# Kernel optimization log

Hardware: AMD Instinct MI355X
Metric: run time of the kernel (lower is better)

Reference implementation:

```python
import jax, jax.numpy as jnp
import numpy as np

NUM_EMBEDDINGS = 1024
EMBEDDING_DIM = 256
COMMITMENT_COST = 0.25
N_TOKENS = 65536


def setup_inputs() -> dict:
    key = jax.random.key(0)
    k1, k2 = jax.random.split(key)
    z = jax.random.normal(k1, (N_TOKENS, EMBEDDING_DIM), dtype=jnp.float32)
    # codebook init as in the module: uniform in [-1/K, 1/K]
    embedding = jax.random.uniform(
        k2, (NUM_EMBEDDINGS, EMBEDDING_DIM),
        minval=-1.0 / NUM_EMBEDDINGS, maxval=1.0 / NUM_EMBEDDINGS,
        dtype=jnp.float32)
    return {"z": z, "embedding": embedding}


def reference(z, embedding):
    # squared euclidean distances: ||z||^2 + ||e||^2 - 2 z.e^T   -> [N, K]
    z_sq = jnp.sum(z ** 2, axis=1, keepdims=True)          # [N, 1]
    emb_sq = jnp.sum(embedding ** 2, axis=1)               # [K]
    dot = jnp.dot(z, embedding.T)                          # [N, K]
    distances = z_sq + emb_sq - 2.0 * dot
    indices = jnp.argmin(distances, axis=1)                # [N]
    z_q = embedding[indices]                               # [N, D] gather
    loss = (jnp.mean((jax.lax.stop_gradient(z) - z_q) ** 2)
            + COMMITMENT_COST * jnp.mean((jax.lax.stop_gradient(z_q) - z) ** 2))
    z_q_st = z + jax.lax.stop_gradient(z_q - z)            # straight-through
    return (z_q_st, loss, indices)
```

## Files before the change

### kernel.cpp

```cpp
#include <hip/hip_runtime.h>
#include <hip/hip_bf16.h>

#define NTOK   65536
#define KCODES 1024
#define DIM    256
#define LOSS_OFF ((size_t)NTOK * DIM)
#define IDX_OFF  (LOSS_OFF + 1)

#define MARGA 2e-4f

#define SC_ZSQ    0
#define SC_LOSS2  131072
#define SC_ESQ    196608
#define SC_ESQNH  197632
#define SC_PART   198656
#define SC_WCNT   198720
#define SC_WCNT2  198721
#define SC_CNTG   198784
#define SC_LISTS  264320
#define SC_WLIST  788608
#define SC_WLIST2 854144
#define SC_EHIMG  858240
#define SC_ZIMG   989312
#define SC_PAIRD  9377920

typedef __attribute__((ext_vector_type(8))) short short8;
typedef __attribute__((ext_vector_type(4))) float f32x4;

__device__ __forceinline__ unsigned f2bf(float x) {
    unsigned u = __float_as_uint(x);
    return (u + 0x7FFFu + ((u >> 16) & 1u)) >> 16;
}

__device__ __forceinline__ void gload16(const void* g, void* l) {
    __builtin_amdgcn_global_load_lds((const __attribute__((address_space(1))) unsigned int*)g,
                                     (__attribute__((address_space(3))) unsigned int*)l,
                                     16, 0, 0);
}

__device__ __forceinline__ float faithful_d(const float* __restrict__ z,
                                            const float* __restrict__ emb,
                                            float zsq, float esq, int tok, int c) {
    const float4* zr = (const float4*)(z + (size_t)tok * DIM);
    const float4* er = (const float4*)(emb + (size_t)c * DIM);
    float acc = 0.f;
#pragma unroll 8
    for (int q = 0; q < 64; ++q) {
        float4 a = zr[q], b = er[q];
        acc = fmaf(a.x, b.x, acc); acc = fmaf(a.y, b.y, acc);
        acc = fmaf(a.z, b.z, acc); acc = fmaf(a.w, b.w, acc);
    }
    float t1 = zsq + esq;
    return t1 - 2.0f * acc;
}

__device__ __forceinline__ float np_rowsq256_wave(const float* row, int sub) {
    const int j = sub & 7, half = sub >> 3;
    const float* a = row + half * 128 + j;
    float r = 0.f;
#pragma unroll
    for (int i = 0; i < 16; ++i) {
        float v = a[i * 8];
        float sq = v * v;
        asm volatile("" : "+v"(sq));
        r += sq;
    }
    float t = r + __shfl_xor(r, 1, 64);
    t = t + __shfl_xor(t, 2, 64);
    t = t + __shfl_xor(t, 4, 64);
    t = t + __shfl_xor(t, 8, 64);
    return t;
}

__global__ __launch_bounds__(256) void vq_prep_esq(const float* __restrict__ emb,
                                                   float* __restrict__ esq,
                                                   float* __restrict__ esqnh,
                                                   int* __restrict__ wcnt,
                                                   int* __restrict__ wcnt2) {
    if (blockIdx.x == 0 && threadIdx.x == 0) { *wcnt = 0; *wcnt2 = 0; }
    int code = blockIdx.x * 16 + (threadIdx.x >> 4);
    int sub = threadIdx.x & 15;
    float tot = np_rowsq256_wave(emb + (size_t)code * DIM, sub);
    if (sub == 0) { esq[code] = tot; esqnh[code] = -0.5f * tot; }
}

__global__ __launch_bounds__(256) void vq_prep_z(const float* __restrict__ z,
                                                 float* __restrict__ zsq,
                                                 unsigned short* __restrict__ zimg) {
    int tok = blockIdx.x * 16 + (threadIdx.x >> 4);
    int sub = threadIdx.x & 15;
    float tot = np_rowsq256_wave(z + (size_t)tok * DIM, sub);
    if (sub == 0) zsq[tok] = tot;

    const float* src = z + (size_t)tok * DIM + sub * 16;
    float4 v0 = *(const float4*)&src[0],  v1 = *(const float4*)&src[4];
    float4 v2 = *(const float4*)&src[8],  v3 = *(const float4*)&src[12];
    uint4 p0, p1;
    p0.x = f2bf(v0.x) | (f2bf(v0.y) << 16);  p0.y = f2bf(v0.z) | (f2bf(v0.w) << 16);
    p0.z = f2bf(v1.x) | (f2bf(v1.y) << 16);  p0.w = f2bf(v1.z) | (f2bf(v1.w) << 16);
    p1.x = f2bf(v2.x) | (f2bf(v2.y) << 16);  p1.y = f2bf(v2.z) | (f2bf(v2.w) << 16);
    p1.z = f2bf(v3.x) | (f2bf(v3.y) << 16);  p1.w = f2bf(v3.z) | (f2bf(v3.w) << 16);

    int bid = tok >> 6, tf = (tok >> 4) & 3, sl = tok & 15;
    int g0 = sub * 2, g1 = g0 + 1;
    size_t rowbase = ((size_t)bid * 4 + tf) * 8;
    char* d0 = (char*)zimg + ((rowbase + (g0 >> 2)) << 10) + (((g0 & 3) * 16 + sl) << 4);
    char* d1 = (char*)zimg + ((rowbase + (g1 >> 2)) << 10) + (((g1 & 3) * 16 + sl) << 4);
    *(uint4*)d0 = p0;
    *(uint4*)d1 = p1;
}

__global__ __launch_bounds__(256) void vq_prep_eimg(const float* __restrict__ emb,
                                                    unsigned short* __restrict__ img) {
    int job = blockIdx.x * 256 + threadIdx.x;
    int code = job >> 3, ks = job & 7;
    int cc = (code >> 6) & 3, lcl = (code >> 8) * 64 + (code & 63);
    const float* src = emb + (size_t)code * DIM + ks * 32;
    char* base = (char*)img + (size_t)(cc * 8 + ks) * 16384;
#pragma unroll
    for (int q = 0; q < 4; ++q) {
        float4 v0 = *(const float4*)&src[q * 8];
        float4 v1 = *(const float4*)&src[q * 8 + 4];
        uint4 p;
        p.x = f2bf(v0.x) | (f2bf(v0.y) << 16);
        p.y = f2bf(v0.z) | (f2bf(v0.w) << 16);
        p.z = f2bf(v1.x) | (f2bf(v1.y) << 16);
        p.w = f2bf(v1.z) | (f2bf(v1.w) << 16);
        *(uint4*)(base + lcl * 64 + ((q * 16) ^ (((lcl >> 1) & 3) << 4))) = p;
    }
}

__global__ __launch_bounds__(256, 2) void vq_gemm(const unsigned short* __restrict__ zimg,
                                                  const unsigned short* __restrict__ img,
                                                  const float* __restrict__ esqnh,
                                                  const float* __restrict__ zsq,
                                                  int* __restrict__ wcnt,
                                                  int* __restrict__ wlist,
                                                  int* __restrict__ cntg,
                                                  int* __restrict__ listsg,
                                                  float* __restrict__ loss2,
                                                  float* __restrict__ dout) {
    __shared__ __align__(16) short eh_s[2][8192];
    __shared__ float a1w_s[4][64];
    __shared__ int   cnt_s[64];
    __shared__ int   lists_s[64 * 16];
    __shared__ float avals_s[64 * 16];

    const int tid = threadIdx.x, bid = blockIdx.x;
    const int w = tid >> 6, l = tid & 63;
    const int t0 = bid * 64;

    short8 zf[4][8];
#pragma unroll
    for (int tf = 0; tf < 4; ++tf)
#pragma unroll
        for (int ks = 0; ks < 8; ++ks)
            zf[tf][ks] = *(const short8*)((const char*)zimg +
                           ((((size_t)bid * 4 + tf) * 8 + ks) << 10) + (size_t)l * 16);

    if (tid < 64) cnt_s[tid] = 0;
    {
        const char* gs = (const char*)img + w * 4096 + (size_t)l * 16;
        char* ld = (char*)&eh_s[0][0] + w * 4096;
#pragma unroll
        for (int i = 0; i < 4; ++i) gload16(gs + i * 1024, ld + i * 1024);
    }
    __syncthreads();

    float m_run[4] = {-3.4e38f, -3.4e38f, -3.4e38f, -3.4e38f};
    f32x4 acc[4][4];

#pragma unroll
    for (int c = 0; c < 4; ++c) {
#pragma unroll
        for (int f = 0; f < 4; ++f) {
            f32x4 e4 = *(const f32x4*)&esqnh[w * 256 + c * 64 + f * 16 + (l >> 4) * 4];
#pragma unroll
            for (int tf = 0; tf < 4; ++tf) acc[f][tf] = e4;
        }
#pragma unroll
        for (int ks = 0; ks < 8; ++ks) {
            int s = c * 8 + ks, buf = s & 1;
            if (s < 31) {
                const char* gs = (const char*)img + (size_t)(s + 1) * 16384 + w * 4096 + (size_t)l * 16;
                char* ld = (char*)&eh_s[buf ^ 1][0] + w * 4096;
#pragma unroll
                for (int i = 0; i < 4; ++i) gload16(gs + i * 1024, ld + i * 1024);
            }
            short8 afr[4];
#pragma unroll
            for (int f = 0; f < 4; ++f) {
                int lcl = w * 64 + f * 16 + (l & 15);
                int byte = lcl * 64 + (((l >> 4) * 16) ^ (((lcl >> 1) & 3) << 4));
                afr[f] = *(const short8*)((const char*)&eh_s[buf][0] + byte);
            }
#pragma unroll
            for (int f = 0; f < 4; ++f)
#pragma unroll
                for (int tf = 0; tf < 4; ++tf)
                    acc[f][tf] = __builtin_amdgcn_mfma_f32_16x16x32_bf16(
                        afr[f], zf[tf][ks], acc[f][tf], 0, 0, 0);
            __syncthreads();
        }
#pragma unroll
        for (int tf = 0; tf < 4; ++tf) {
            float m0 = fmaxf(fmaxf(acc[0][tf][0], acc[0][tf][1]), fmaxf(acc[0][tf][2], acc[0][tf][3]));
            float m1 = fmaxf(fmaxf(acc[1][tf][0], acc[1][tf][1]), fmaxf(acc[1][tf][2], acc[1][tf][3]));
            float m2 = fmaxf(fmaxf(acc[2][tf][0], acc[2][tf][1]), fmaxf(acc[2][tf][2], acc[2][tf][3]));
            float m3 = fmaxf(fmaxf(acc[3][tf][0], acc[3][tf][1]), fmaxf(acc[3][tf][2], acc[3][tf][3]));
            float tm = fmaxf(fmaxf(m0, m1), fmaxf(m2, m3));
            tm = fmaxf(tm, __shfl_xor(tm, 16, 64));
            tm = fmaxf(tm, __shfl_xor(tm, 32, 64));
            if (l < 16) a1w_s[w][tf * 16 + l] = tm;
        }
        __syncthreads();
#pragma unroll
        for (int tf = 0; tf < 4; ++tf) {
            int tokl = tf * 16 + (l & 15);
            float gm = fmaxf(fmaxf(a1w_s[0][tokl], a1w_s[1][tokl]),
                             fmaxf(a1w_s[2][tokl], a1w_s[3][tokl]));
            m_run[tf] = fmaxf(m_run[tf], gm);
            float thr = m_run[tf] - MARGA;
#pragma unroll
            for (int f = 0; f < 4; ++f)
#pragma unroll
                for (int r = 0; r < 4; ++r) {
                    float a = acc[f][tf][r];
                    if (a >= thr) {
                        int code = w * 256 + c * 64 + f * 16 + (l >> 4) * 4 + r;
                        int pos = atomicAdd(&cnt_s[tokl], 1);
                        if (pos < 16) {
                            lists_s[tokl * 16 + pos] = code;
                            avals_s[tokl * 16 + pos] = a;
                        }
                    }
                }
        }
    }

    __syncthreads();

    if (tid < 64) {
        int t = t0 + tid;
        int tfsel = tid >> 4;
        float a1v = (tfsel == 0) ? m_run[0] : (tfsel == 1) ? m_run[1]
                  : (tfsel == 2) ? m_run[2] : m_run[3];
        int ct_raw = cnt_s[tid];
        if (ct_raw > 16) {
            int pos = atomicAdd(wcnt, 1);
            wlist[pos] = t;
            cntg[t] = 999;
        } else {
            float thr = a1v - MARGA;
            int kept = 0, first = 0;
            for (int i = 0; i < ct_raw; ++i) {
                float av = avals_s[tid * 16 + i];
                if (av >= thr) {
                    int code = lists_s[tid * 16 + i];
                    if (kept == 0) first = code;
                    if (kept < 8) listsg[(size_t)t * 8 + kept] = code;
                    ++kept;
                }
            }
            if (kept == 1) {
                dout[IDX_OFF + t] = (float)first;
                loss2[t] = fmaf(-2.f, a1v, zsq[t]);
            } else {
                int pos = atomicAdd(wcnt, 1);
                wlist[pos] = t;
                cntg[t] = (kept > 8) ? 999 : kept;
            }
        }
    }
}

__global__ __launch_bounds__(256) void vq_pairs(const float* __restrict__ z,
                                                const float* __restrict__ emb,
                                                const float* __restrict__ zsq,
                                                const float* __restrict__ esq,
                                                const int* __restrict__ wcnt,
                                                const int* __restrict__ wlist,
                                                const int* __restrict__ cntg,
                                                const int* __restrict__ listsg,
                                                int* __restrict__ wcnt2,
                                                int* __restrict__ wlist2,
                                                float* __restrict__ paird) {
    const int n = wcnt[0];
    const int total = 8 * n;
    for (int p = blockIdx.x * 256 + threadIdx.x; p < total; p += 2048 * 256) {
        int q = p >> 3, slot = p & 7;
        int tok = wlist[q];
        int ct = cntg[tok];
        if (ct == 0 || ct > 8) {
            if (slot == 0) {
                int pos = atomicAdd(wcnt2, 1);
                if (pos < 4096) wlist2[pos] = tok;
            }
            continue;
        }
        if (slot >= ct) continue;
        int code = listsg[(size_t)tok * 8 + slot];
        paird[p] = faithful_d(z, emb, zsq[tok], esq[code], tok, code);
    }
}

__global__ __launch_bounds__(256) void vq_pick(const float* __restrict__ paird,
                                               const int* __restrict__ wcnt,
                                               const int* __restrict__ wlist,
                                               const int* __restrict__ cntg,
                                               const int* __restrict__ listsg,
                                               float* __restrict__ loss2,
                                               float* __restrict__ dout) {
    const int n = wcnt[0];
    for (int q = blockIdx.x * 256 + threadIdx.x; q < n; q += 256 * 256) {
        int tok = wlist[q];
        int ct = cntg[tok];
        if (ct == 0 || ct > 8) continue;
        float db = paird[q * 8];
        int cb = listsg[(size_t)tok * 8];
        for (int i = 1; i < ct; ++i) {
            float d = paird[q * 8 + i];
            int c = listsg[(size_t)tok * 8 + i];
            if (d < db || (d == db && c < cb)) { db = d; cb = c; }
        }
        dout[IDX_OFF + tok] = (float)cb;
        loss2[tok] = db;
    }
}

__global__ __launch_bounds__(256) void vq_decide_scan(const float* __restrict__ z,
                                                      const float* __restrict__ emb,
                                                      const float* __restrict__ zsq,
                                                      const float* __restrict__ esq,
                                                      const int* __restrict__ wcnt2,
                                                      const int* __restrict__ wlist2,
                                                      float* __restrict__ loss2,
                                                      float* __restrict__ dout) {
    __shared__ __align__(16) float zrow[DIM];
    __shared__ float dred[256];
    __shared__ int   ired[256];
    int n = wcnt2[0];
    if (n > 4096) n = 4096;
    const int tid = threadIdx.x;
    for (int job = blockIdx.x; job < n; job += 128) {
        int tok = wlist2[job];
        __syncthreads();
        if (tid < 64) ((float4*)zrow)[tid] = ((const float4*)(z + (size_t)tok * DIM))[tid];
        __syncthreads();
        float zq = zsq[tok];
        float a0 = 0.f, a1v = 0.f, a2 = 0.f, a3 = 0.f;
        const float4* e0 = (const float4*)(emb + (size_t)(tid      ) * DIM);
        const float4* e1 = (const float4*)(emb + (size_t)(tid + 256) * DIM);
        const float4* e2 = (const float4*)(emb + (size_t)(tid + 512) * DIM);
        const float4* e3 = (const float4*)(emb + (size_t)(tid + 768) * DIM);
#pragma unroll
        for (int seg = 0; seg < 4; ++seg) {
#pragma unroll
            for (int qq = 0; qq < 16; ++qq) {
                float4 a = ((float4*)zrow)[seg * 16 + qq];
                float4 b0 = e0[seg * 16 + qq], b1 = e1[seg * 16 + qq];
                float4 b2 = e2[seg * 16 + qq], b3 = e3[seg * 16 + qq];
                a0 = fmaf(a.x, b0.x, a0); a0 = fmaf(a.y, b0.y, a0);
                a0 = fmaf(a.z, b0.z, a0); a0 = fmaf(a.w, b0.w, a0);
                a1v = fmaf(a.x, b1.x, a1v); a1v = fmaf(a.y, b1.y, a1v);
                a1v = fmaf(a.z, b1.z, a1v); a1v = fmaf(a.w, b1.w, a1v);
                a2 = fmaf(a.x, b2.x, a2); a2 = fmaf(a.y, b2.y, a2);
                a2 = fmaf(a.z, b2.z, a2); a2 = fmaf(a.w, b2.w, a2);
                a3 = fmaf(a.x, b3.x, a3); a3 = fmaf(a.y, b3.y, a3);
                a3 = fmaf(a.z, b3.z, a3); a3 = fmaf(a.w, b3.w, a3);
            }
        }
        float d0 = (zq + esq[tid      ]) - 2.0f * a0;
        float d1 = (zq + esq[tid + 256]) - 2.0f * a1v;
        float d2 = (zq + esq[tid + 512]) - 2.0f * a2;
        float d3 = (zq + esq[tid + 768]) - 2.0f * a3;
        float db = d0; int cb = tid;
        if (d1 < db) { db = d1; cb = tid + 256; }
        if (d2 < db) { db = d2; cb = tid + 512; }
        if (d3 < db) { db = d3; cb = tid + 768; }
        dred[tid] = db; ired[tid] = cb;
        __syncthreads();
        for (int step = 128; step >= 1; step >>= 1) {
            if (tid < step) {
                float od = dred[tid + step]; int oi = ired[tid + step];
                if (od < dred[tid] || (od == dred[tid] && oi < ired[tid])) {
                    dred[tid] = od; ired[tid] = oi;
                }
            }
            __syncthreads();
        }
        if (tid == 0) {
            dout[IDX_OFF + tok] = (float)ired[0];
            loss2[tok] = dred[0];
        }
    }
}

__global__ __launch_bounds__(256) void vq_sum(const float* __restrict__ loss2,
                                              float* __restrict__ part) {
    __shared__ float ws[4];
    float s = 0.f;
#pragma unroll
    for (int q = 0; q < 4; ++q)
        s += loss2[blockIdx.x * 1024 + q * 256 + threadIdx.x];
#pragma unroll
    for (int m = 1; m < 64; m <<= 1) s += __shfl_xor(s, m, 64);
    if ((threadIdx.x & 63) == 0) ws[threadIdx.x >> 6] = s;
    __syncthreads();
    if (threadIdx.x == 0) part[blockIdx.x] = ws[0] + ws[1] + ws[2] + ws[3];
}

__global__ __launch_bounds__(64) void vq_final(const float* __restrict__ part,
                                               float* __restrict__ dout) {
    double s = (double)part[threadIdx.x];
#pragma unroll
    for (int m = 1; m < 64; m <<= 1) s += __shfl_xor(s, m, 64);
    if (threadIdx.x == 0) dout[LOSS_OFF] = (float)(s * 1.25 / 16777216.0);
}

__global__ __launch_bounds__(256) void vq_gather(const float* __restrict__ emb,
                                                 float* __restrict__ dout) {
    const int w = threadIdx.x >> 6, l = threadIdx.x & 63;
    for (int tok = blockIdx.x * 4 + w; tok < NTOK; tok += 2048 * 4) {
        int widx = (int)dout[IDX_OFF + tok];
        float4 ev = *(const float4*)&emb[(size_t)widx * DIM + l * 4];
        *(float4*)&dout[(size_t)tok * DIM + l * 4] = ev;
    }
}

extern "C" void kernel_launch(void* const* d_in, const int* in_sizes, int n_in,
                              void* d_out, int out_size, void* d_ws, size_t ws_size,
                              hipStream_t stream) {
    const float* z   = (const float*)d_in[0];
    const float* emb = (const float*)d_in[1];
    float* out = (float*)d_out;

    float* zsq   = out + SC_ZSQ;
    float* loss2 = out + SC_LOSS2;
    float* esq   = out + SC_ESQ;
    float* esqnh = out + SC_ESQNH;
    float* part  = out + SC_PART;
    int*   wcnt  = (int*)(out + SC_WCNT);
    int*   wcnt2 = (int*)(out + SC_WCNT2);
    int*   cntg  = (int*)(out + SC_CNTG);
    int*   listsg= (int*)(out + SC_LISTS);
    int*   wlist = (int*)(out + SC_WLIST);
    int*   wlist2= (int*)(out + SC_WLIST2);
    float* paird = out + SC_PAIRD;
    unsigned short* img  = (unsigned short*)(out + SC_EHIMG);
    unsigned short* zimg = (unsigned short*)(out + SC_ZIMG);

    vq_prep_esq <<<64,   256, 0, stream>>>(emb, esq, esqnh, wcnt, wcnt2);
    vq_prep_z   <<<4096, 256, 0, stream>>>(z, zsq, zimg);
    vq_prep_eimg<<<32,   256, 0, stream>>>(emb, img);
    vq_gemm     <<<1024, 256, 0, stream>>>(zimg, img, esqnh, zsq, wcnt, wlist, cntg, listsg, loss2, out);
    vq_pairs    <<<2048, 256, 0, stream>>>(z, emb, zsq, esq, wcnt, wlist, cntg, listsg, wcnt2, wlist2, paird);
    vq_pick     <<<256,  256, 0, stream>>>(paird, wcnt, wlist, cntg, listsg, loss2, out);
    vq_decide_scan<<<128, 256, 0, stream>>>(z, emb, zsq, esq, wcnt2, wlist2, loss2, out);
    vq_sum      <<<64,   256, 0, stream>>>(loss2, part);
    vq_final    <<<1,    64,  0, stream>>>(part, out);
    vq_gather   <<<2048, 256, 0, stream>>>(emb, out);
}
```

Baseline: 136.8 us.

## Double LDS stage depth in VQ GEMM, fuse embedding prep kernels, shrink pairs grid

The GEMM main loop now loads two k-slices of the codebook into shared memory per stage, so the loop runs 16 iterations instead of 32 and each iteration does 32 MFMAs between barriers. This halves the number of __syncthreads and prefetch points, but doubles LDS use per block, which may affect occupancy at two blocks per CU. The esq and bf16 codebook image prep kernels are merged into one launch to save a kernel launch. The pairs kernel grid drops from 2048 to 512 blocks and now strides by gridDim.

```diff
diff --git a/kernel.cpp b/kernel.cpp
--- a/kernel.cpp
+++ b/kernel.cpp
@@ -72,16 +72,37 @@
     return t;
 }
 
-__global__ __launch_bounds__(256) void vq_prep_esq(const float* __restrict__ emb,
+__global__ __launch_bounds__(256) void vq_prep_emb(const float* __restrict__ emb,
                                                    float* __restrict__ esq,
                                                    float* __restrict__ esqnh,
+                                                   unsigned short* __restrict__ img,
                                                    int* __restrict__ wcnt,
                                                    int* __restrict__ wcnt2) {
     if (blockIdx.x == 0 && threadIdx.x == 0) { *wcnt = 0; *wcnt2 = 0; }
-    int code = blockIdx.x * 16 + (threadIdx.x >> 4);
-    int sub = threadIdx.x & 15;
-    float tot = np_rowsq256_wave(emb + (size_t)code * DIM, sub);
-    if (sub == 0) { esq[code] = tot; esqnh[code] = -0.5f * tot; }
+    {
+        int code = blockIdx.x * 16 + (threadIdx.x >> 4);
+        int sub = threadIdx.x & 15;
+        float tot = np_rowsq256_wave(emb + (size_t)code * DIM, sub);
+        if (sub == 0) { esq[code] = tot; esqnh[code] = -0.5f * tot; }
+    }
+    if (threadIdx.x < 128) {
+        int job = blockIdx.x * 128 + threadIdx.x;
+        int code = job >> 3, ks = job & 7;
+        int cc = (code >> 6) & 3, lcl = (code >> 8) * 64 + (code & 63);
+        const float* src = emb + (size_t)code * DIM + ks * 32;
+        char* base = (char*)img + (size_t)(cc * 8 + ks) * 16384;
+#pragma unroll
+        for (int q = 0; q < 4; ++q) {
+            float4 v0 = *(const float4*)&src[q * 8];
+            float4 v1 = *(const float4*)&src[q * 8 + 4];
+            uint4 p;
+            p.x = f2bf(v0.x) | (f2bf(v0.y) << 16);
+            p.y = f2bf(v0.z) | (f2bf(v0.w) << 16);
+            p.z = f2bf(v1.x) | (f2bf(v1.y) << 16);
+            p.w = f2bf(v1.z) | (f2bf(v1.w) << 16);
+            *(uint4*)(base + lcl * 64 + ((q * 16) ^ (((lcl >> 1) & 3) << 4))) = p;
+        }
+    }
 }
 
 __global__ __launch_bounds__(256) void vq_prep_z(const float* __restrict__ z,
@@ -108,26 +129,6 @@
     char* d1 = (char*)zimg + ((rowbase + (g1 >> 2)) << 10) + (((g1 & 3) * 16 + sl) << 4);
     *(uint4*)d0 = p0;
     *(uint4*)d1 = p1;
-}
-
-__global__ __launch_bounds__(256) void vq_prep_eimg(const float* __restrict__ emb,
-                                                    unsigned short* __restrict__ img) {
-    int job = blockIdx.x * 256 + threadIdx.x;
-    int code = job >> 3, ks = job & 7;
-    int cc = (code >> 6) & 3, lcl = (code >> 8) * 64 + (code & 63);
-    const float* src = emb + (size_t)code * DIM + ks * 32;
-    char* base = (char*)img + (size_t)(cc * 8 + ks) * 16384;
-#pragma unroll
-    for (int q = 0; q < 4; ++q) {
-        float4 v0 = *(const float4*)&src[q * 8];
-        float4 v1 = *(const float4*)&src[q * 8 + 4];
-        uint4 p;
-        p.x = f2bf(v0.x) | (f2bf(v0.y) << 16);
-        p.y = f2bf(v0.z) | (f2bf(v0.w) << 16);
-        p.z = f2bf(v1.x) | (f2bf(v1.y) << 16);
-        p.w = f2bf(v1.z) | (f2bf(v1.w) << 16);
-        *(uint4*)(base + lcl * 64 + ((q * 16) ^ (((lcl >> 1) & 3) << 4))) = p;
-    }
 }
 
 __global__ __launch_bounds__(256, 2) void vq_gemm(const unsigned short* __restrict__ zimg,
@@ -140,7 +141,7 @@
                                                   int* __restrict__ listsg,
                                                   float* __restrict__ loss2,
                                                   float* __restrict__ dout) {
-    __shared__ __align__(16) short eh_s[2][8192];
+    __shared__ __align__(16) short eh_s[2][16384];
     __shared__ float a1w_s[4][64];
     __shared__ int   cnt_s[64];
     __shared__ int   lists_s[64 * 16];
@@ -164,6 +165,10 @@
         char* ld = (char*)&eh_s[0][0] + w * 4096;
 #pragma unroll
         for (int i = 0; i < 4; ++i) gload16(gs + i * 1024, ld + i * 1024);
+        const char* gs1 = gs + 16384;
+        char* ld1 = ld + 16384;
+#pragma unroll
+        for (int i = 0; i < 4; ++i) gload16(gs1 + i * 1024, ld1 + i * 1024);
     }
     __syncthreads();
 
@@ -171,22 +176,27 @@
     f32x4 acc[4][4];
 
 #pragma unroll
-    for (int c = 0; c < 4; ++c) {
-#pragma unroll
-        for (int f = 0; f < 4; ++f) {
-            f32x4 e4 = *(const f32x4*)&esqnh[w * 256 + c * 64 + f * 16 + (l >> 4) * 4];
-#pragma unroll
-            for (int tf = 0; tf < 4; ++tf) acc[f][tf] = e4;
-        }
-#pragma unroll
-        for (int ks = 0; ks < 8; ++ks) {
-            int s = c * 8 + ks, buf = s & 1;
-            if (s < 31) {
-                const char* gs = (const char*)img + (size_t)(s + 1) * 16384 + w * 4096 + (size_t)l * 16;
-                char* ld = (char*)&eh_s[buf ^ 1][0] + w * 4096;
-#pragma unroll
-                for (int i = 0; i < 4; ++i) gload16(gs + i * 1024, ld + i * 1024);
-            }
+    for (int p = 0; p < 16; ++p) {
+        const int c = p >> 2, q = p & 3, buf = p & 1;
+        if (q == 0) {
+#pragma unroll
+            for (int f = 0; f < 4; ++f) {
+                f32x4 e4 = *(const f32x4*)&esqnh[w * 256 + c * 64 + f * 16 + (l >> 4) * 4];
+#pragma unroll
+                for (int tf = 0; tf < 4; ++tf) acc[f][tf] = e4;
+            }
+        }
+        if (p < 15) {
+            const char* gs = (const char*)img + (size_t)(p + 1) * 32768 + w * 4096 + (size_t)l * 16;
+            char* ld = (char*)&eh_s[buf ^ 1][0] + w * 4096;
+#pragma unroll
+            for (int i = 0; i < 4; ++i) gload16(gs + i * 1024, ld + i * 1024);
+            const char* gs1 = gs + 16384;
+            char* ld1 = ld + 16384;
+#pragma unroll
+            for (int i = 0; i < 4; ++i) gload16(gs1 + i * 1024, ld1 + i * 1024);
+        }
+        {
             short8 afr[4];
 #pragma unroll
             for (int f = 0; f < 4; ++f) {
@@ -199,42 +209,60 @@
 #pragma unroll
                 for (int tf = 0; tf < 4; ++tf)
                     acc[f][tf] = __builtin_amdgcn_mfma_f32_16x16x32_bf16(
-                        afr[f], zf[tf][ks], acc[f][tf], 0, 0, 0);
+                        afr[f], zf[tf][2 * q], acc[f][tf], 0, 0, 0);
+        }
+        {
+            short8 afr[4];
+#pragma unroll
+            for (int f = 0; f < 4; ++f) {
+                int lcl = w * 64 + f * 16 + (l & 15);
+                int byte = 16384 + lcl * 64 + (((l >> 4) * 16) ^ (((lcl >> 1) & 3) << 4));
+                afr[f] = *(const short8*)((const char*)&eh_s[buf][0] + byte);
+            }
+#pragma unroll
+            for (int f = 0; f < 4; ++f)
+#pragma unroll
+                for (int tf = 0; tf < 4; ++tf)
+                    acc[f][tf] = __builtin_amdgcn_mfma_f32_16x16x32_bf16(
+                        afr[f], zf[tf][2 * q + 1], acc[f][tf], 0, 0, 0);
+        }
+        __syncthreads();
+
+        if (q == 3) {
+#pragma unroll
+            for (int tf = 0; tf < 4; ++tf) {
+                float m0 = fmaxf(fmaxf(acc[0][tf][0], acc[0][tf][1]), fmaxf(acc[0][tf][2], acc[0][tf][3]));
+                float m1 = fmaxf(fmaxf(acc[1][tf][0], acc[1][tf][1]), fmaxf(acc[1][tf][2], acc[1][tf][3]));
+                float m2 = fmaxf(fmaxf(acc[2][tf][0], acc[2][tf][1]), fmaxf(acc[2][tf][2], acc[2][tf][3]));
+                float m3 = fmaxf(fmaxf(acc[3][tf][0], acc[3][tf][1]), fmaxf(acc[3][tf][2], acc[3][tf][3]));
+                float tm = fmaxf(fmaxf(m0, m1), fmaxf(m2, m3));
+                tm = fmaxf(tm, __shfl_xor(tm, 16, 64));
+                tm = fmaxf(tm, __shfl_xor(tm, 32, 64));
+                if (l < 16) a1w_s[w][tf * 16 + l] = tm;
+            }
             __syncthreads();
-        }
-#pragma unroll
-        for (int tf = 0; tf < 4; ++tf) {
-            float m0 = fmaxf(fmaxf(acc[0][tf][0], acc[0][tf][1]), fmaxf(acc[0][tf][2], acc[0][tf][3]));
-            float m1 = fmaxf(fmaxf(acc[1][tf][0], acc[1][tf][1]), fmaxf(acc[1][tf][2], acc[1][tf][3]));
-            float m2 = fmaxf(fmaxf(acc[2][tf][0], acc[2][tf][1]), fmaxf(acc[2][tf][2], acc[2][tf][3]));
-            float m3 = fmaxf(fmaxf(acc[3][tf][0], acc[3][tf][1]), fmaxf(acc[3][tf][2], acc[3][tf][3]));
-            float tm = fmaxf(fmaxf(m0, m1), fmaxf(m2, m3));
-            tm = fmaxf(tm, __shfl_xor(tm, 16, 64));
-            tm = fmaxf(tm, __shfl_xor(tm, 32, 64));
-            if (l < 16) a1w_s[w][tf * 16 + l] = tm;
-        }
-        __syncthreads();
-#pragma unroll
-        for (int tf = 0; tf < 4; ++tf) {
-            int tokl = tf * 16 + (l & 15);
-            float gm = fmaxf(fmaxf(a1w_s[0][tokl], a1w_s[1][tokl]),
-                             fmaxf(a1w_s[2][tokl], a1w_s[3][tokl]));
-            m_run[tf] = fmaxf(m_run[tf], gm);
-            float thr = m_run[tf] - MARGA;
-#pragma unroll
-            for (int f = 0; f < 4; ++f)
-#pragma unroll
-                for (int r = 0; r < 4; ++r) {
-                    float a = acc[f][tf][r];
-                    if (a >= thr) {
-                        int code = w * 256 + c * 64 + f * 16 + (l >> 4) * 4 + r;
-                        int pos = atomicAdd(&cnt_s[tokl], 1);
-                        if (pos < 16) {
-                            lists_s[tokl * 16 + pos] = code;
-                            avals_s[tokl * 16 + pos] = a;
+#pragma unroll
+            for (int tf = 0; tf < 4; ++tf) {
+                int tokl = tf * 16 + (l & 15);
+                float gm = fmaxf(fmaxf(a1w_s[0][tokl], a1w_s[1][tokl]),
+                                 fmaxf(a1w_s[2][tokl], a1w_s[3][tokl]));
+                m_run[tf] = fmaxf(m_run[tf], gm);
+                float thr = m_run[tf] - MARGA;
+#pragma unroll
+                for (int f = 0; f < 4; ++f)
+#pragma unroll
+                    for (int r = 0; r < 4; ++r) {
+                        float a = acc[f][tf][r];
+                        if (a >= thr) {
+                            int code = w * 256 + c * 64 + f * 16 + (l >> 4) * 4 + r;
+                            int pos = atomicAdd(&cnt_s[tokl], 1);
+                            if (pos < 16) {
+                                lists_s[tokl * 16 + pos] = code;
+                                avals_s[tokl * 16 + pos] = a;
+                            }
                         }
                     }
-                }
+            }
         }
     }
 
@@ -287,7 +315,7 @@
                                                 float* __restrict__ paird) {
     const int n = wcnt[0];
     const int total = 8 * n;
-    for (int p = blockIdx.x * 256 + threadIdx.x; p < total; p += 2048 * 256) {
+    for (int p = blockIdx.x * 256 + threadIdx.x; p < total; p += gridDim.x * 256) {
         int q = p >> 3, slot = p & 7;
         int tok = wlist[q];
         int ct = cntg[tok];
@@ -312,7 +340,7 @@
                                                float* __restrict__ loss2,
                                                float* __restrict__ dout) {
     const int n = wcnt[0];
-    for (int q = blockIdx.x * 256 + threadIdx.x; q < n; q += 256 * 256) {
+    for (int q = blockIdx.x * 256 + threadIdx.x; q < n; q += gridDim.x * 256) {
         int tok = wlist[q];
         int ct = cntg[tok];
         if (ct == 0 || ct > 8) continue;
@@ -450,11 +478,10 @@
     unsigned short* img  = (unsigned short*)(out + SC_EHIMG);
     unsigned short* zimg = (unsigned short*)(out + SC_ZIMG);
 
-    vq_prep_esq <<<64,   256, 0, stream>>>(emb, esq, esqnh, wcnt, wcnt2);
+    vq_prep_emb <<<64,   256, 0, stream>>>(emb, esq, esqnh, img, wcnt, wcnt2);
     vq_prep_z   <<<4096, 256, 0, stream>>>(z, zsq, zimg);
-    vq_prep_eimg<<<32,   256, 0, stream>>>(emb, img);
     vq_gemm     <<<1024, 256, 0, stream>>>(zimg, img, esqnh, zsq, wcnt, wlist, cntg, listsg, loss2, out);
-    vq_pairs    <<<2048, 256, 0, stream>>>(z, emb, zsq, esq, wcnt, wlist, cntg, listsg, wcnt2, wlist2, paird);
+    vq_pairs    <<<512,  256, 0, stream>>>(z, emb, zsq, esq, wcnt, wlist, cntg, listsg, wcnt2, wlist2, paird);
     vq_pick     <<<256,  256, 0, stream>>>(paird, wcnt, wlist, cntg, listsg, loss2, out);
     vq_decide_scan<<<128, 256, 0, stream>>>(z, emb, zsq, esq, wcnt2, wlist2, loss2, out);
     vq_sum      <<<64,   256, 0, stream>>>(loss2, part);
```

Result: faster. 128.8 us (-5.8%).
